# Kernel tuning notes

Measured on AMD Instinct MI355X. Metric: run time of the kernel, lower is better.

Reference implementation:

```python
import jax, jax.numpy as jnp
import numpy as np

ETA = 0.1
DT = 1.0
H, DH = 8, 64


def setup_inputs() -> dict:
    key = jax.random.key(0)
    ks = jax.random.split(key, 7)
    B, N, D = 4, 2048, 1024
    s = 0.02
    return {
        "x": jax.random.normal(ks[0], (B, N, D), dtype=jnp.float32),
        "gamma": jax.random.uniform(ks[1], (B, N), dtype=jnp.float32),
        "state": jnp.zeros((B, H, DH, DH), dtype=jnp.float32),
        "Wq": (jax.random.normal(ks[2], (D, H * DH), dtype=jnp.float32) * s),
        "Wk": (jax.random.normal(ks[3], (D, H * DH), dtype=jnp.float32) * s),
        "Wv": (jax.random.normal(ks[4], (D, H * DH), dtype=jnp.float32) * s),
        "Wo": (jax.random.normal(ks[5], (H * DH, D), dtype=jnp.float32) * s),
        "bo": jnp.zeros((D,), dtype=jnp.float32),
    }


def reference(x, gamma, state, Wq, Wk, Wv, Wo, bo):
    B, N, D = x.shape
    # projections -> (N, B, H, DH) for scan over time
    q = (x @ Wq).reshape(B, N, H, DH).transpose(1, 0, 2, 3)
    k = (x @ Wk).reshape(B, N, H, DH).transpose(1, 0, 2, 3)
    v = (x @ Wv).reshape(B, N, H, DH).transpose(1, 0, 2, 3)
    # decay = exp(-clamp(gamma*dt, max=10)) -> (N, B)
    decay = jnp.exp(-jnp.minimum(gamma * DT, 10.0)).T

    def step(st, inp):
        q_t, k_t, v_t, d_t = inp  # (B,H,DH),(B,H,DH),(B,H,DH),(B,)
        # W_new = exp(-Gamma*dt) * stop_grad(W_old) + eta * k^T v
        st_new = d_t[:, None, None, None] * jax.lax.stop_gradient(st) \
                 + ETA * jnp.einsum('bhi,bhj->bhij', k_t, v_t)
        y_t = jnp.einsum('bhij,bhj->bhi', st_new, q_t)  # (B,H,DH)
        return st_new, y_t

    state_final, ys = jax.lax.scan(step, state, (q, k, v, decay))
    # ys: (N, B, H, DH) -> (B, N, H*DH)
    y = ys.transpose(1, 0, 2, 3).reshape(B, N, H * DH)
    out = y @ Wo + bo
    return out, state_final
```

## Files before the change

kernel.cpp:

```cpp
#include <hip/hip_runtime.h>

#define ETA 0.1f
#define BATCH 4
#define SEQ 2048
#define DMODEL 1024
#define NH 8
#define DHEAD 64
#define HD 512
#define QKVW 1536
#define CH 64
#define NCH (SEQ / CH)

typedef float f32x4 __attribute__((ext_vector_type(4)));
typedef short short8 __attribute__((ext_vector_type(8)));
typedef short short4v __attribute__((ext_vector_type(4)));

static __device__ __forceinline__ ushort f2bf(float f) {
  union { float f; unsigned u; } x; x.f = f;
  unsigned r = (x.u + 0x7fffu + ((x.u >> 16) & 1u)) >> 16;
  return (ushort)r;
}
static __device__ __forceinline__ float bf2f(ushort u) {
  union { unsigned u; float f; } x; x.u = ((unsigned)u) << 16;
  return x.f;
}

#define GLDS16(g, l)                                                    \
  __builtin_amdgcn_global_load_lds(                                     \
      (const __attribute__((address_space(1))) unsigned int*)(const void*)(g), \
      (__attribute__((address_space(3))) unsigned int*)(void*)(l), 16, 0, 0)

__global__ __launch_bounds__(256) void conv_kernel(
    const float* __restrict__ x, const float* __restrict__ Wq,
    const float* __restrict__ Wk, const float* __restrict__ Wv,
    const float* __restrict__ Wo, ushort* __restrict__ xb,
    ushort* __restrict__ Wt, ushort* __restrict__ Wot) {
  const int tid = threadIdx.x;
  __shared__ float T[32][33];
  if (blockIdx.x < 2048) {
    size_t i = ((size_t)blockIdx.x * 256 + tid) * 16;
    ushort t[16];
#pragma unroll
    for (int u = 0; u < 4; ++u) {
      f32x4 v = *(const f32x4*)&x[i + u * 4];
#pragma unroll
      for (int e = 0; e < 4; ++e) t[u * 4 + e] = f2bf(v[e]);
    }
    *(short8*)&xb[i] = *(short8*)&t[0];
    *(short8*)&xb[i + 8] = *(short8*)&t[8];
    return;
  }
  const int idx = blockIdx.x - 2048;
  const int m = idx >> 9;
  const int bx = idx & 511;
  const float* src;
  ushort* dst;
  int srcN, dstK, k0, n0, rowOff;
  if (m < 3) {
    src = (m == 0) ? Wq : ((m == 1) ? Wk : Wv);
    srcN = 512; dstK = 1024;
    k0 = (bx >> 4) << 5; n0 = (bx & 15) << 5;
    dst = Wt; rowOff = m * 512;
  } else {
    src = Wo; srcN = 1024; dstK = 512;
    k0 = (bx >> 5) << 5; n0 = (bx & 31) << 5;
    dst = Wot; rowOff = 0;
  }
  const int r = tid >> 3, c4 = (tid & 7) << 2;
  f32x4 v = *(const f32x4*)&src[(size_t)(k0 + r) * srcN + n0 + c4];
  T[r][c4 + 0] = v[0]; T[r][c4 + 1] = v[1];
  T[r][c4 + 2] = v[2]; T[r][c4 + 3] = v[3];
  __syncthreads();
  short4v o;
#pragma unroll
  for (int e = 0; e < 4; ++e) o[e] = (short)f2bf(T[c4 + e][r]);
  *(short4v*)&dst[(size_t)(rowOff + n0 + r) * dstK + k0 + c4] = o;
}

template <bool OUT_BF16>
__global__ __launch_bounds__(256, 3) void gemm_bt_kernel(
    const ushort* __restrict__ A, const ushort* __restrict__ Bt,
    void* __restrict__ Cv, const float* __restrict__ bias,
    int M, int N, int K) {
  const int tiles_n = N >> 7;
  const int nwg = gridDim.x;
  const int bid = blockIdx.x;
  const int swz = (bid & 7) * (nwg >> 3) + (bid >> 3);
  const int bm = swz / tiles_n;
  const int bn = swz % tiles_n;
  const int tid = threadIdx.x;
  const int w = tid >> 6, lane = tid & 63;
  const int wr = w >> 1, wc = w & 1;
  const int fr = lane & 15, fq = lane >> 4;

  __shared__ ushort As[3][128][32];
  __shared__ ushort Bs[3][128][32];

  f32x4 acc[4][4];
#pragma unroll
  for (int mi = 0; mi < 4; ++mi)
#pragma unroll
    for (int ni = 0; ni < 4; ++ni) acc[mi][ni] = f32x4{0.f, 0.f, 0.f, 0.f};

  const int lw = lane >> 2;
  const int scz = ((lane & 3) ^ ((lane >> 3) & 3)) << 3;
  const ushort* ga = A + (size_t)(bm * 128 + w * 32 + lw) * K + scz;
  const ushort* gb = Bt + (size_t)(bn * 128 + w * 32 + lw) * K + scz;
  const size_t rstep = (size_t)16 * K;

  const int nt = K >> 5;

#pragma unroll
  for (int pt = 0; pt < 2; ++pt) {
    ushort* la = &As[pt][w * 32][0];
    ushort* lb = &Bs[pt][w * 32][0];
    GLDS16(ga + pt * 32, la);
    GLDS16(ga + pt * 32 + rstep, la + 512);
    GLDS16(gb + pt * 32, lb);
    GLDS16(gb + pt * 32 + rstep, lb + 512);
  }

  const int fqs8 = (fq ^ ((fr >> 1) & 3)) * 8;

  for (int t = 0; t < nt; ++t) {
    if (t < nt - 1) {
      asm volatile("s_waitcnt vmcnt(4) lgkmcnt(0)\n\ts_barrier" ::: "memory");
    } else {
      asm volatile("s_waitcnt vmcnt(0) lgkmcnt(0)\n\ts_barrier" ::: "memory");
    }
    if (t + 2 < nt) {
      const int sb = (t + 2) % 3;
      const int kt = (t + 2) << 5;
      ushort* la = &As[sb][w * 32][0];
      ushort* lb = &Bs[sb][w * 32][0];
      GLDS16(ga + kt, la);
      GLDS16(ga + kt + rstep, la + 512);
      GLDS16(gb + kt, lb);
      GLDS16(gb + kt + rstep, lb + 512);
    }
    const int cb = t % 3;
    short8 a[4], b[4];
#pragma unroll
    for (int mi = 0; mi < 4; ++mi)
      a[mi] = *(const short8*)&As[cb][wr * 64 + mi * 16 + fr][fqs8];
#pragma unroll
    for (int ni = 0; ni < 4; ++ni)
      b[ni] = *(const short8*)&Bs[cb][wc * 64 + ni * 16 + fr][fqs8];
#pragma unroll
    for (int mi = 0; mi < 4; ++mi)
#pragma unroll
      for (int ni = 0; ni < 4; ++ni)
        acc[mi][ni] = __builtin_amdgcn_mfma_f32_16x16x32_bf16(
            a[mi], b[ni], acc[mi][ni], 0, 0, 0);
  }

#pragma unroll
  for (int ni = 0; ni < 4; ++ni) {
    const int gc = bn * 128 + wc * 64 + ni * 16 + fr;
    float badd = (!OUT_BF16 && bias) ? bias[gc] : 0.f;
#pragma unroll
    for (int mi = 0; mi < 4; ++mi) {
#pragma unroll
      for (int r = 0; r < 4; ++r) {
        const int gr = bm * 128 + wr * 64 + mi * 16 + fq * 4 + r;
        if (OUT_BF16) {
          ((ushort*)Cv)[(size_t)gr * N + gc] = f2bf(acc[mi][ni][r]);
        } else {
          ((float*)Cv)[(size_t)gr * N + gc] = acc[mi][ni][r] + badd;
        }
      }
    }
  }
}

__global__ __launch_bounds__(256) void intraS_kernel(
    const ushort* __restrict__ qkv, const float* __restrict__ gamma,
    ushort* __restrict__ S, float* __restrict__ clb) {
  const int bx = blockIdx.x;
  const int c = bx & (NCH - 1);
  const int h = (bx >> 5) & (NH - 1);
  const int b = bx >> 8;
  const int tid = threadIdx.x;
  const int w = tid >> 6, lane = tid & 63;
  const int fr = lane & 15, fq = lane >> 4;

  __shared__ ushort KT[64][72];
  __shared__ ushort VT[64][72];
  __shared__ float cumS[64];

  const int p = tid >> 2, d0 = (tid & 3) * 16;
  const ushort* base = &qkv[((size_t)b * SEQ + c * CH + p) * QKVW + h * 64 + d0];
  short8 k0 = *(const short8*)(base + 512);
  short8 k1 = *(const short8*)(base + 520);
  short8 v0 = *(const short8*)(base + 1024);
  short8 v1 = *(const short8*)(base + 1032);

  {
    float g = gamma[(size_t)b * SEQ + c * CH + lane];
    float prod = expf(-fminf(g, 10.f));
#pragma unroll
    for (int off = 1; off < 64; off <<= 1) {
      float o = __shfl_up(prod, off);
      if (lane >= off) prod *= o;
    }
    cumS[lane] = prod;
  }
  __syncthreads();

  {
    const float rc = 1.f / cumS[p];
#pragma unroll
    for (int j = 0; j < 8; ++j) {
      KT[d0 + j][p] = (ushort)k0[j];
      KT[d0 + 8 + j][p] = (ushort)k1[j];
      VT[d0 + j][p] = f2bf(bf2f((ushort)v0[j]) * rc);
      VT[d0 + 8 + j][p] = f2bf(bf2f((ushort)v1[j]) * rc);
    }
  }
  __syncthreads();

  const float scl = ETA * cumS[63];
  const int arow = w * 16 + fr;
  short8 ka0 = *(const short8*)&KT[arow][fq * 8];
  short8 ka1 = *(const short8*)&KT[arow][32 + fq * 8];
  ushort* Sp = &S[(((size_t)(b * NH + h)) * NCH + c) << 12];
#pragma unroll
  for (int cf = 0; cf < 4; ++cf) {
    short8 bv0 = *(const short8*)&VT[cf * 16 + fr][fq * 8];
    short8 bv1 = *(const short8*)&VT[cf * 16 + fr][32 + fq * 8];
    f32x4 accS = {0.f, 0.f, 0.f, 0.f};
    accS = __builtin_amdgcn_mfma_f32_16x16x32_bf16(ka0, bv0, accS, 0, 0, 0);
    accS = __builtin_amdgcn_mfma_f32_16x16x32_bf16(ka1, bv1, accS, 0, 0, 0);
#pragma unroll
    for (int r = 0; r < 4; ++r) {
      int row = w * 16 + fq * 4 + r;
      int col = cf * 16 + fr;
      Sp[row * 64 + col] = f2bf(accS[r] * scl);
    }
  }
  if (tid == 0 && h == 0) clb[b * NCH + c] = cumS[63];
}

__global__ __launch_bounds__(256) void prop_kernel(
    const float* __restrict__ state0, const ushort* __restrict__ S,
    const float* __restrict__ clb, ushort* __restrict__ stash,
    float* __restrict__ state_out) {
  const int bh = blockIdx.x >> 2, rg = blockIdx.x & 3;
  const int b = bh >> 3;
  const int tid = threadIdx.x;
  const int i = rg * 16 + (tid >> 4);
  const int j0 = (tid & 15) * 4;
  const size_t off = ((size_t)bh * 64 + i) * 64 + j0;
  const size_t coff = (size_t)i * 64 + j0;

  f32x4 st = *(const f32x4*)&state0[off];
#pragma unroll 4
  for (int c = 0; c < NCH; ++c) {
    const size_t base = (((size_t)bh * NCH + c) << 12) + coff;
    short4v sv;
#pragma unroll
    for (int e = 0; e < 4; ++e) sv[e] = (short)f2bf(st[e]);
    *(short4v*)&stash[base] = sv;
    short4v s = *(const short4v*)&S[base];
    float clv = clb[b * NCH + c];
#pragma unroll
    for (int e = 0; e < 4; ++e) st[e] = st[e] * clv + bf2f((ushort)s[e]);
  }
  *(f32x4*)&state_out[off] = st;
}

__global__ __launch_bounds__(256) void intraY_kernel(
    const ushort* __restrict__ qkv, const float* __restrict__ gamma,
    const ushort* __restrict__ stash, ushort* __restrict__ ybf) {
  const int bx = blockIdx.x;
  const int c = bx & (NCH - 1);
  const int h = (bx >> 5) & (NH - 1);
  const int b = bx >> 8;
  const int tid = threadIdx.x;
  const int w = tid >> 6, lane = tid & 63;
  const int fr = lane & 15, fq = lane >> 4;

  __shared__ ushort Qs[64][72];
  __shared__ ushort Vs[64][72];
  __shared__ ushort KT[64][72];
  __shared__ ushort Ps[64][72];
  __shared__ ushort Bst[64][72];
  __shared__ float cumS[64];

  const int p = tid >> 2, d0 = (tid & 3) * 16;
  const ushort* base = &qkv[((size_t)b * SEQ + c * CH + p) * QKVW + h * 64 + d0];
  short8 q0 = *(const short8*)base;
  short8 q1 = *(const short8*)(base + 8);
  short8 k0 = *(const short8*)(base + 512);
  short8 k1 = *(const short8*)(base + 520);
  short8 v0 = *(const short8*)(base + 1024);
  short8 v1 = *(const short8*)(base + 1032);
  const size_t sb = ((((size_t)(b * NH + h)) * NCH + c) << 12) + (size_t)p * 64 + d0;
  short8 s0 = *(const short8*)&stash[sb];
  short8 s1 = *(const short8*)&stash[sb + 8];

  {
    float g = gamma[(size_t)b * SEQ + c * CH + lane];
    float prod = expf(-fminf(g, 10.f));
#pragma unroll
    for (int off = 1; off < 64; off <<= 1) {
      float o = __shfl_up(prod, off);
      if (lane >= off) prod *= o;
    }
    cumS[lane] = prod;
  }
  __syncthreads();

  {
    const float cp = cumS[p];
    const float rc = 1.f / cp;
    ushort tq[16], tv[16];
#pragma unroll
    for (int j = 0; j < 8; ++j) {
      tq[j]     = f2bf(bf2f((ushort)q0[j]) * cp);
      tq[8 + j] = f2bf(bf2f((ushort)q1[j]) * cp);
      tv[j]     = f2bf(bf2f((ushort)v0[j]) * rc);
      tv[8 + j] = f2bf(bf2f((ushort)v1[j]) * rc);
      KT[d0 + j][p] = (ushort)k0[j];
      KT[d0 + 8 + j][p] = (ushort)k1[j];
    }
    *(short8*)&Qs[p][d0] = *(short8*)&tq[0];
    *(short8*)&Qs[p][d0 + 8] = *(short8*)&tq[8];
    *(short8*)&Vs[p][d0] = *(short8*)&tv[0];
    *(short8*)&Vs[p][d0 + 8] = *(short8*)&tv[8];
    *(short8*)&Bst[p][d0] = s0;
    *(short8*)&Bst[p][d0 + 8] = s1;
  }
  __syncthreads();

  const int arow = w * 16 + fr;
  short8 a0 = *(const short8*)&Qs[arow][fq * 8];
  short8 a1 = *(const short8*)&Qs[arow][32 + fq * 8];

#pragma unroll
  for (int cf = 0; cf < 4; ++cf) {
    f32x4 acc = {0.f, 0.f, 0.f, 0.f};
    if (cf <= w) {
      short8 b0 = *(const short8*)&Vs[cf * 16 + fr][fq * 8];
      short8 b1 = *(const short8*)&Vs[cf * 16 + fr][32 + fq * 8];
      acc = __builtin_amdgcn_mfma_f32_16x16x32_bf16(a0, b0, acc, 0, 0, 0);
      acc = __builtin_amdgcn_mfma_f32_16x16x32_bf16(a1, b1, acc, 0, 0, 0);
    }
#pragma unroll
    for (int r = 0; r < 4; ++r) {
      int pi = w * 16 + fq * 4 + r, si = cf * 16 + fr;
      Ps[pi][si] = f2bf((si <= pi) ? acc[r] * ETA : 0.f);
    }
  }
  __syncthreads();

  short8 p0 = *(const short8*)&Ps[arow][fq * 8];
  short8 p1 = *(const short8*)&Ps[arow][32 + fq * 8];
  const size_t yrow0 = (size_t)b * SEQ + c * CH;
#pragma unroll
  for (int cf = 0; cf < 4; ++cf) {
    f32x4 accY = {0.f, 0.f, 0.f, 0.f};
    short8 bs0 = *(const short8*)&Bst[cf * 16 + fr][fq * 8];
    short8 bs1 = *(const short8*)&Bst[cf * 16 + fr][32 + fq * 8];
    accY = __builtin_amdgcn_mfma_f32_16x16x32_bf16(a0, bs0, accY, 0, 0, 0);
    accY = __builtin_amdgcn_mfma_f32_16x16x32_bf16(a1, bs1, accY, 0, 0, 0);
    short8 bk0 = *(const short8*)&KT[cf * 16 + fr][fq * 8];
    short8 bk1 = *(const short8*)&KT[cf * 16 + fr][32 + fq * 8];
    accY = __builtin_amdgcn_mfma_f32_16x16x32_bf16(p0, bk0, accY, 0, 0, 0);
    accY = __builtin_amdgcn_mfma_f32_16x16x32_bf16(p1, bk1, accY, 0, 0, 0);
#pragma unroll
    for (int r = 0; r < 4; ++r) {
      int row = w * 16 + fq * 4 + r;
      int col = cf * 16 + fr;
      ybf[(yrow0 + row) * HD + h * 64 + col] = f2bf(accY[r]);
    }
  }
}

extern "C" void kernel_launch(void* const* d_in, const int* in_sizes, int n_in,
                              void* d_out, int out_size, void* d_ws, size_t ws_size,
                              hipStream_t stream) {
  const float* x      = (const float*)d_in[0];
  const float* gamma  = (const float*)d_in[1];
  const float* state0 = (const float*)d_in[2];
  const float* Wq     = (const float*)d_in[3];
  const float* Wk     = (const float*)d_in[4];
  const float* Wv     = (const float*)d_in[5];
  const float* Wo     = (const float*)d_in[6];
  const float* bo     = (const float*)d_in[7];

  float* out = (float*)d_out;
  float* state_out = out + (size_t)BATCH * SEQ * DMODEL;

  const int M = BATCH * SEQ;

  ushort* xb  = (ushort*)d_ws;
  ushort* wt  = xb + (size_t)M * DMODEL;
  ushort* wot = wt + (size_t)QKVW * DMODEL;
  ushort* qkv = wot + (size_t)DMODEL * HD;
  ushort* ybf = qkv + (size_t)M * QKVW;
  ushort* Sb  = ybf + (size_t)M * HD;
  ushort* stash = Sb + (size_t)BATCH * NH * NCH * 4096;
  float*  clb   = (float*)(stash + (size_t)BATCH * NH * NCH * 4096);

  dim3 blk(256);

  conv_kernel<<<dim3(4096), blk, 0, stream>>>(x, Wq, Wk, Wv, Wo, xb, wt, wot);

  gemm_bt_kernel<true><<<dim3((M / 128) * (QKVW / 128)), blk, 0, stream>>>(
      xb, wt, qkv, nullptr, M, QKVW, DMODEL);

  intraS_kernel<<<dim3(BATCH * NH * NCH), blk, 0, stream>>>(
      qkv, gamma, Sb, clb);
  prop_kernel<<<dim3(BATCH * NH * 4), blk, 0, stream>>>(
      state0, Sb, clb, stash, state_out);
  intraY_kernel<<<dim3(BATCH * NH * NCH), blk, 0, stream>>>(
      qkv, gamma, stash, ybf);

  gemm_bt_kernel<false><<<dim3((M / 128) * (DMODEL / 128)), blk, 0, stream>>>(
      ybf, wot, out, bo, M, DMODEL, HD);
}
```

Baseline: 92.39 us.

## Fuse inter-chunk state propagation into intraY via weighted prefix sums

```diff
diff --git a/kernel.cpp b/kernel.cpp
--- a/kernel.cpp
+++ b/kernel.cpp
@@ -241,41 +241,16 @@
   if (tid == 0 && h == 0) clb[b * NCH + c] = cumS[63];
 }
 
-__global__ __launch_bounds__(256) void prop_kernel(
-    const float* __restrict__ state0, const ushort* __restrict__ S,
-    const float* __restrict__ clb, ushort* __restrict__ stash,
-    float* __restrict__ state_out) {
-  const int bh = blockIdx.x >> 2, rg = blockIdx.x & 3;
-  const int b = bh >> 3;
-  const int tid = threadIdx.x;
-  const int i = rg * 16 + (tid >> 4);
-  const int j0 = (tid & 15) * 4;
-  const size_t off = ((size_t)bh * 64 + i) * 64 + j0;
-  const size_t coff = (size_t)i * 64 + j0;
-
-  f32x4 st = *(const f32x4*)&state0[off];
-#pragma unroll 4
-  for (int c = 0; c < NCH; ++c) {
-    const size_t base = (((size_t)bh * NCH + c) << 12) + coff;
-    short4v sv;
-#pragma unroll
-    for (int e = 0; e < 4; ++e) sv[e] = (short)f2bf(st[e]);
-    *(short4v*)&stash[base] = sv;
-    short4v s = *(const short4v*)&S[base];
-    float clv = clb[b * NCH + c];
-#pragma unroll
-    for (int e = 0; e < 4; ++e) st[e] = st[e] * clv + bf2f((ushort)s[e]);
-  }
-  *(f32x4*)&state_out[off] = st;
-}
-
 __global__ __launch_bounds__(256) void intraY_kernel(
     const ushort* __restrict__ qkv, const float* __restrict__ gamma,
-    const ushort* __restrict__ stash, ushort* __restrict__ ybf) {
+    const ushort* __restrict__ S, const float* __restrict__ clb,
+    const float* __restrict__ state0, ushort* __restrict__ ybf,
+    float* __restrict__ state_out) {
   const int bx = blockIdx.x;
   const int c = bx & (NCH - 1);
   const int h = (bx >> 5) & (NH - 1);
   const int b = bx >> 8;
+  const int bh = b * NH + h;
   const int tid = threadIdx.x;
   const int w = tid >> 6, lane = tid & 63;
   const int fr = lane & 15, fq = lane >> 4;
@@ -286,6 +261,7 @@
   __shared__ ushort Ps[64][72];
   __shared__ ushort Bst[64][72];
   __shared__ float cumS[64];
+  __shared__ float prodS[32];
 
   const int p = tid >> 2, d0 = (tid & 3) * 16;
   const ushort* base = &qkv[((size_t)b * SEQ + c * CH + p) * QKVW + h * 64 + d0];
@@ -295,9 +271,6 @@
   short8 k1 = *(const short8*)(base + 520);
   short8 v0 = *(const short8*)(base + 1024);
   short8 v1 = *(const short8*)(base + 1032);
-  const size_t sb = ((((size_t)(b * NH + h)) * NCH + c) << 12) + (size_t)p * 64 + d0;
-  short8 s0 = *(const short8*)&stash[sb];
-  short8 s1 = *(const short8*)&stash[sb + 8];
 
   {
     float g = gamma[(size_t)b * SEQ + c * CH + lane];
@@ -309,12 +282,63 @@
     }
     cumS[lane] = prod;
   }
-  __syncthreads();
+  if (tid < 32) {
+    float pl = (tid < c) ? clb[b * NCH + tid] : 1.f;
+    float prod = pl;
+#pragma unroll
+    for (int off = 1; off < 32; off <<= 1) {
+      float o = __shfl_down(prod, off);
+      if (tid + off < 32) prod *= o;
+    }
+    prodS[tid] = prod;
+  }
+  __syncthreads();
+
+  float sa[16], sa2[16];
+  {
+    const float pre0 = prodS[0];
+    const float* s0p = &state0[((size_t)bh * 64 + p) * 64 + d0];
+#pragma unroll
+    for (int u = 0; u < 4; ++u) {
+      f32x4 sv = *(const f32x4*)&s0p[u * 4];
+#pragma unroll
+      for (int e = 0; e < 4; ++e) { sa[u * 4 + e] = pre0 * sv[e]; sa2[u * 4 + e] = 0.f; }
+    }
+    const ushort* Sbase = S + (((size_t)bh * NCH) << 12) + (size_t)p * 64 + d0;
+    int cc = 0;
+    for (; cc + 1 < c; cc += 2) {
+      short8 ea = *(const short8*)(Sbase + ((size_t)cc << 12));
+      short8 eb = *(const short8*)(Sbase + ((size_t)cc << 12) + 8);
+      short8 fa = *(const short8*)(Sbase + ((size_t)(cc + 1) << 12));
+      short8 fb = *(const short8*)(Sbase + ((size_t)(cc + 1) << 12) + 8);
+      float wa = prodS[cc + 1];
+      float wb = (cc + 2 < 32) ? prodS[cc + 2] : 1.f;
+#pragma unroll
+      for (int j = 0; j < 8; ++j) {
+        sa[j]      += wa * bf2f((ushort)ea[j]);
+        sa[8 + j]  += wa * bf2f((ushort)eb[j]);
+        sa2[j]     += wb * bf2f((ushort)fa[j]);
+        sa2[8 + j] += wb * bf2f((ushort)fb[j]);
+      }
+    }
+    if (cc < c) {
+      short8 ea = *(const short8*)(Sbase + ((size_t)cc << 12));
+      short8 eb = *(const short8*)(Sbase + ((size_t)cc << 12) + 8);
+      float wa = (cc + 1 < 32) ? prodS[cc + 1] : 1.f;
+#pragma unroll
+      for (int j = 0; j < 8; ++j) {
+        sa[j]     += wa * bf2f((ushort)ea[j]);
+        sa[8 + j] += wa * bf2f((ushort)eb[j]);
+      }
+    }
+#pragma unroll
+    for (int j = 0; j < 16; ++j) sa[j] += sa2[j];
+  }
 
   {
     const float cp = cumS[p];
     const float rc = 1.f / cp;
-    ushort tq[16], tv[16];
+    ushort tq[16], tv[16], ts[16];
 #pragma unroll
     for (int j = 0; j < 8; ++j) {
       tq[j]     = f2bf(bf2f((ushort)q0[j]) * cp);
@@ -324,12 +348,14 @@
       KT[d0 + j][p] = (ushort)k0[j];
       KT[d0 + 8 + j][p] = (ushort)k1[j];
     }
+#pragma unroll
+    for (int j = 0; j < 16; ++j) ts[j] = f2bf(sa[j]);
     *(short8*)&Qs[p][d0] = *(short8*)&tq[0];
     *(short8*)&Qs[p][d0 + 8] = *(short8*)&tq[8];
     *(short8*)&Vs[p][d0] = *(short8*)&tv[0];
     *(short8*)&Vs[p][d0 + 8] = *(short8*)&tv[8];
-    *(short8*)&Bst[p][d0] = s0;
-    *(short8*)&Bst[p][d0 + 8] = s1;
+    *(short8*)&Bst[p][d0] = *(short8*)&ts[0];
+    *(short8*)&Bst[p][d0 + 8] = *(short8*)&ts[8];
   }
   __syncthreads();
 
@@ -373,6 +399,25 @@
       int row = w * 16 + fq * 4 + r;
       int col = cf * 16 + fr;
       ybf[(yrow0 + row) * HD + h * 64 + col] = f2bf(accY[r]);
+    }
+  }
+
+  if (c == NCH - 1) {
+    const float clv = clb[b * NCH + c];
+    const ushort* Sc = S + (((size_t)bh * NCH + c) << 12) + (size_t)p * 64 + d0;
+    short8 ea = *(const short8*)Sc;
+    short8 eb = *(const short8*)(Sc + 8);
+    float* so = &state_out[((size_t)bh * 64 + p) * 64 + d0];
+#pragma unroll
+    for (int u = 0; u < 4; ++u) {
+      f32x4 ov;
+#pragma unroll
+      for (int e = 0; e < 4; ++e) {
+        int j = u * 4 + e;
+        float sj = (j < 8) ? bf2f((ushort)ea[j]) : bf2f((ushort)eb[j - 8]);
+        ov[e] = clv * sa[j] + sj;
+      }
+      *(f32x4*)&so[u * 4] = ov;
     }
   }
 }
@@ -400,8 +445,7 @@
   ushort* qkv = wot + (size_t)DMODEL * HD;
   ushort* ybf = qkv + (size_t)M * QKVW;
   ushort* Sb  = ybf + (size_t)M * HD;
-  ushort* stash = Sb + (size_t)BATCH * NH * NCH * 4096;
-  float*  clb   = (float*)(stash + (size_t)BATCH * NH * NCH * 4096);
+  float*  clb = (float*)(Sb + (size_t)BATCH * NH * NCH * 4096);
 
   dim3 blk(256);
 
@@ -412,10 +456,8 @@
 
   intraS_kernel<<<dim3(BATCH * NH * NCH), blk, 0, stream>>>(
       qkv, gamma, Sb, clb);
-  prop_kernel<<<dim3(BATCH * NH * 4), blk, 0, stream>>>(
-      state0, Sb, clb, stash, state_out);
   intraY_kernel<<<dim3(BATCH * NH * NCH), blk, 0, stream>>>(
-      qkv, gamma, stash, ybf);
+      qkv, gamma, Sb, clb, state0, ybf, state_out);
 
   gemm_bt_kernel<false><<<dim3((M / 128) * (DMODEL / 128)), blk, 0, stream>>>(
       ybf, wot, out, bo, M, DMODEL, HD);
```

Result: slower. 95.87 us (+3.8%).

## Fuse fp32-to-bf16 conversion of x into the QKV projection GEMM

Applied to the files above, without the earlier changes.

```diff
diff --git a/kernel.cpp b/kernel.cpp
--- a/kernel.cpp
+++ b/kernel.cpp
@@ -1,4 +1,5 @@
 #include <hip/hip_runtime.h>
+#include <hip/hip_bf16.h>
 
 #define ETA 0.1f
 #define BATCH 4
@@ -24,6 +25,11 @@
   union { unsigned u; float f; } x; x.u = ((unsigned)u) << 16;
   return x.f;
 }
+static __device__ __forceinline__ ushort f2bh(float f) {
+  union { __hip_bfloat16 h; ushort u; } x;
+  x.h = __float2bfloat16(f);
+  return x.u;
+}
 
 #define GLDS16(g, l)                                                    \
   __builtin_amdgcn_global_load_lds(                                     \
@@ -31,26 +37,12 @@
       (__attribute__((address_space(3))) unsigned int*)(void*)(l), 16, 0, 0)
 
 __global__ __launch_bounds__(256) void conv_kernel(
-    const float* __restrict__ x, const float* __restrict__ Wq,
-    const float* __restrict__ Wk, const float* __restrict__ Wv,
-    const float* __restrict__ Wo, ushort* __restrict__ xb,
+    const float* __restrict__ Wq, const float* __restrict__ Wk,
+    const float* __restrict__ Wv, const float* __restrict__ Wo,
     ushort* __restrict__ Wt, ushort* __restrict__ Wot) {
   const int tid = threadIdx.x;
   __shared__ float T[32][33];
-  if (blockIdx.x < 2048) {
-    size_t i = ((size_t)blockIdx.x * 256 + tid) * 16;
-    ushort t[16];
-#pragma unroll
-    for (int u = 0; u < 4; ++u) {
-      f32x4 v = *(const f32x4*)&x[i + u * 4];
-#pragma unroll
-      for (int e = 0; e < 4; ++e) t[u * 4 + e] = f2bf(v[e]);
-    }
-    *(short8*)&xb[i] = *(short8*)&t[0];
-    *(short8*)&xb[i + 8] = *(short8*)&t[8];
-    return;
-  }
-  const int idx = blockIdx.x - 2048;
+  const int idx = blockIdx.x;
   const int m = idx >> 9;
   const int bx = idx & 511;
   const float* src;
@@ -75,6 +67,125 @@
 #pragma unroll
   for (int e = 0; e < 4; ++e) o[e] = (short)f2bf(T[c4 + e][r]);
   *(short4v*)&dst[(size_t)(rowOff + n0 + r) * dstK + k0 + c4] = o;
+}
+
+__global__ __launch_bounds__(256, 3) void gemm_qkv_kernel(
+    const float* __restrict__ Af, const ushort* __restrict__ Bt,
+    ushort* __restrict__ C, int M, int N, int K) {
+  const int tiles_n = N >> 7;
+  const int nwg = gridDim.x;
+  const int bid = blockIdx.x;
+  const int swz = (bid & 7) * (nwg >> 3) + (bid >> 3);
+  const int bm = swz / tiles_n;
+  const int bn = swz % tiles_n;
+  const int tid = threadIdx.x;
+  const int w = tid >> 6, lane = tid & 63;
+  const int wr = w >> 1, wc = w & 1;
+  const int fr = lane & 15, fq = lane >> 4;
+
+  __shared__ ushort As[3][128][32];
+  __shared__ ushort Bs[3][128][32];
+
+  f32x4 acc[4][4];
+#pragma unroll
+  for (int mi = 0; mi < 4; ++mi)
+#pragma unroll
+    for (int ni = 0; ni < 4; ++ni) acc[mi][ni] = f32x4{0.f, 0.f, 0.f, 0.f};
+
+  const int sr = tid >> 1;
+  const int sh = (tid & 1) << 4;
+  const float* gaf = Af + (size_t)(bm * 128 + sr) * K + sh;
+  const int sw = (sr >> 1) & 3;
+  const int ch0 = (((tid & 1) << 1)) ^ sw;
+  const int ch1 = (((tid & 1) << 1) + 1) ^ sw;
+  const int lw = lane >> 2;
+  const int scz = ((lane & 3) ^ ((lane >> 3) & 3)) << 3;
+  const ushort* gb = Bt + (size_t)(bn * 128 + w * 32 + lw) * K + scz;
+  const size_t rstep = (size_t)16 * K;
+
+  const int nt = K >> 5;
+  const int fqs8 = (fq ^ ((fr >> 1) & 3)) * 8;
+
+  f32x4 pA0, pA1, pA2, pA3;
+  f32x4 qA0, qA1, qA2, qA3;
+
+#define LOADA(s0, s1, s2, s3, tt)                                       \
+  { const float* ap = gaf + (size_t)(tt) * 32;                          \
+    s0 = *(const f32x4*)ap;       s1 = *(const f32x4*)(ap + 4);         \
+    s2 = *(const f32x4*)(ap + 8); s3 = *(const f32x4*)(ap + 12); }
+#define GLDB(tt)                                                        \
+  { ushort* lb = &Bs[(tt) % 3][w * 32][0];                              \
+    GLDS16(gb + (tt) * 32, lb);                                         \
+    GLDS16(gb + (tt) * 32 + rstep, lb + 512); }
+#define WRITEA(s0, s1, s2, s3, tt)                                      \
+  { ushort ta[16];                                                      \
+    ta[0]=f2bh(s0[0]); ta[1]=f2bh(s0[1]); ta[2]=f2bh(s0[2]); ta[3]=f2bh(s0[3]); \
+    ta[4]=f2bh(s1[0]); ta[5]=f2bh(s1[1]); ta[6]=f2bh(s1[2]); ta[7]=f2bh(s1[3]); \
+    ta[8]=f2bh(s2[0]); ta[9]=f2bh(s2[1]); ta[10]=f2bh(s2[2]); ta[11]=f2bh(s2[3]); \
+    ta[12]=f2bh(s3[0]); ta[13]=f2bh(s3[1]); ta[14]=f2bh(s3[2]); ta[15]=f2bh(s3[3]); \
+    *(short8*)&As[(tt) % 3][sr][ch0 * 8] = *(short8*)&ta[0];            \
+    *(short8*)&As[(tt) % 3][sr][ch1 * 8] = *(short8*)&ta[8]; }
+#define COMPUTE(tt)                                                     \
+  { const int cb = (tt) % 3;                                            \
+    short8 a[4], b[4];                                                  \
+    _Pragma("unroll")                                                   \
+    for (int mi = 0; mi < 4; ++mi)                                      \
+      a[mi] = *(const short8*)&As[cb][wr * 64 + mi * 16 + fr][fqs8];    \
+    _Pragma("unroll")                                                   \
+    for (int ni = 0; ni < 4; ++ni)                                      \
+      b[ni] = *(const short8*)&Bs[cb][wc * 64 + ni * 16 + fr][fqs8];    \
+    _Pragma("unroll")                                                   \
+    for (int mi = 0; mi < 4; ++mi)                                      \
+      _Pragma("unroll")                                                 \
+      for (int ni = 0; ni < 4; ++ni)                                    \
+        acc[mi][ni] = __builtin_amdgcn_mfma_f32_16x16x32_bf16(          \
+            a[mi], b[ni], acc[mi][ni], 0, 0, 0); }
+
+  LOADA(pA0, pA1, pA2, pA3, 0);
+  GLDB(0);
+  LOADA(qA0, qA1, qA2, qA3, 1);
+  GLDB(1);
+  asm volatile("s_waitcnt vmcnt(8)" ::: "memory");
+  WRITEA(pA0, pA1, pA2, pA3, 0);
+  LOADA(pA0, pA1, pA2, pA3, 2);
+
+  for (int t = 0; t < nt; t += 2) {
+    if (t < nt - 3) {
+      asm volatile("s_waitcnt vmcnt(6) lgkmcnt(0)\n\ts_barrier" ::: "memory");
+    } else {
+      asm volatile("s_waitcnt vmcnt(0) lgkmcnt(0)\n\ts_barrier" ::: "memory");
+    }
+    if (t + 1 < nt) WRITEA(qA0, qA1, qA2, qA3, t + 1);
+    if (t + 3 < nt) LOADA(qA0, qA1, qA2, qA3, t + 3);
+    if (t + 2 < nt) GLDB(t + 2);
+    COMPUTE(t);
+    if (t + 1 < nt - 3) {
+      asm volatile("s_waitcnt vmcnt(6) lgkmcnt(0)\n\ts_barrier" ::: "memory");
+    } else {
+      asm volatile("s_waitcnt vmcnt(0) lgkmcnt(0)\n\ts_barrier" ::: "memory");
+    }
+    if (t + 2 < nt) WRITEA(pA0, pA1, pA2, pA3, t + 2);
+    if (t + 4 < nt) LOADA(pA0, pA1, pA2, pA3, t + 4);
+    if (t + 3 < nt) GLDB(t + 3);
+    COMPUTE(t + 1);
+  }
+#undef LOADA
+#undef GLDB
+#undef WRITEA
+#undef COMPUTE
+
+#pragma unroll
+  for (int ni = 0; ni < 4; ++ni) {
+    const int gc = bn * 128 + wc * 64 + ni * 16 + fr;
+#pragma unroll
+    for (int mi = 0; mi < 4; ++mi) {
+#pragma unroll
+      for (int r = 0; r < 4; ++r) {
+        const int gr = bm * 128 + wr * 64 + mi * 16 + fq * 4 + r;
+        C[(size_t)gr * N + gc] = f2bf(acc[mi][ni][r]);
+      }
+    }
+  }
 }
 
 template <bool OUT_BF16>
@@ -394,8 +505,7 @@
 
   const int M = BATCH * SEQ;
 
-  ushort* xb  = (ushort*)d_ws;
-  ushort* wt  = xb + (size_t)M * DMODEL;
+  ushort* wt  = (ushort*)d_ws;
   ushort* wot = wt + (size_t)QKVW * DMODEL;
   ushort* qkv = wot + (size_t)DMODEL * HD;
   ushort* ybf = qkv + (size_t)M * QKVW;
@@ -405,10 +515,10 @@
 
   dim3 blk(256);
 
-  conv_kernel<<<dim3(4096), blk, 0, stream>>>(x, Wq, Wk, Wv, Wo, xb, wt, wot);
-
-  gemm_bt_kernel<true><<<dim3((M / 128) * (QKVW / 128)), blk, 0, stream>>>(
-      xb, wt, qkv, nullptr, M, QKVW, DMODEL);
+  conv_kernel<<<dim3(2048), blk, 0, stream>>>(Wq, Wk, Wv, Wo, wt, wot);
+
+  gemm_qkv_kernel<<<dim3((M / 128) * (QKVW / 128)), blk, 0, stream>>>(
+      x, wt, qkv, M, QKVW, DMODEL);
 
   intraS_kernel<<<dim3(BATCH * NH * NCH), blk, 0, stream>>>(
       qkv, gamma, Sb, clb);
```

After: 94.37 us. +2.1%, slower.
